# Kernel tuning notes

Hardware: AMD Instinct MI355X
Metric: run time of the kernel (lower is better)

Reference implementation:

```python
import jax, jax.numpy as jnp
import numpy as np
import jax.lax as lax


def _log_bf_np(z, s2, s0):
    # Bayes factor per feature; s0 is the prior precision tau_0[l,k] (scalar)
    s0_inv = 1.0 / s0
    s2ps0inv = s2 + s0_inv
    return 0.5 * (jnp.log(s2) - jnp.log(s2ps0inv) + z ** 2 * (s0_inv / s2ps0inv))


def setup_inputs() -> dict:
    key = jax.random.key(0)
    ks = jax.random.split(key, 8)
    n, p, z, l = 1000, 50000, 20, 10
    data = jax.random.normal(ks[0], (n, p), jnp.float32)
    mean_z = jax.random.normal(ks[1], (n, z), jnp.float32)
    # factor second moment must be PSD with strictly positive diagonal (E_zzk > 0)
    mean_zz = (mean_z.T @ mean_z) / n + jnp.eye(z, dtype=jnp.float32)
    mean_w = jax.random.normal(ks[2], (l, z, p), jnp.float32) * 0.01
    var_w = jax.random.uniform(ks[3], (l, z), jnp.float32, minval=0.1, maxval=1.0)
    alpha = jax.random.uniform(ks[4], (l, z, p), jnp.float32)
    alpha = alpha / jnp.sum(alpha, axis=-1, keepdims=True)
    tau = jnp.asarray(1.5, jnp.float32)
    tau_0 = jax.random.uniform(ks[5], (l, z), jnp.float32, minval=0.5, maxval=2.0)
    pi = jax.random.uniform(ks[6], (z, p), jnp.float32, minval=0.5, maxval=1.5)
    pi = pi / jnp.sum(pi, axis=-1, keepdims=True)
    return {"data": data, "mean_z": mean_z, "mean_zz": mean_zz, "mean_w": mean_w,
            "var_w": var_w, "alpha": alpha, "tau": tau, "tau_0": tau_0, "pi": pi}


def reference(data, mean_z, mean_zz, mean_w, var_w, alpha, tau, tau_0, pi):
    """LoadingModel.update: sequential CAVI over factors (k) and single effects (l).
    mean_w/alpha: [l, z, p]; var_w/tau_0: [l, z]; pi: [z, p]; data: [n, p]; mean_z: [n, z].
    Returns updated (mean_w, var_w, alpha)."""
    l_dim, z_dim, p_dim = mean_w.shape
    # collapsed loading moments: W[k, :] = sum_l mean_w[l,k,:] * alpha[l,k,:]
    W = jnp.sum(mean_w * alpha, axis=0)            # [z, p]
    ZtX = mean_z.T @ data                           # [z, p] (precompute of mean_z[:,k] @ data)
    log_pi = jnp.log(pi)                            # [z, p]

    def factor_step(carry, kdx):
        W, mean_w, var_w, alpha = carry
        E_zzk = mean_zz[kdx, kdx]
        Wk = W[kdx]                                 # [p]
        # Wnk.T @ E_zpzk over j != k  ==  mean_zz[kdx] @ W - E_zzk * Wk (avoids the gather)
        RtZk = ZtX[kdx] - (mean_zz[kdx] @ W - E_zzk * Wk)   # [p]
        log_pi_k = log_pi[kdx]
        s2_s = 1.0 / (E_zzk * tau)
        zs_scale = jnp.sqrt(E_zzk * tau) / E_zzk

        def effect_step(Wk, xs):
            mw_l, a_l, t0_l = xs                    # [p], [p], scalar
            Wkl = Wk - mw_l * a_l                   # remove effect l from residual fit
            E_RtZk = RtZk - E_zzk * Wkl             # [p]
            var_new = jnp.reciprocal(tau * E_zzk + t0_l)   # scalar
            mean_new = tau * var_new * E_RtZk       # [p]
            Z_s = E_RtZk * zs_scale
            log_bf = _log_bf_np(Z_s, s2_s, t0_l)
            alpha_new = jax.nn.softmax(log_pi_k + log_bf)
            Wk_new = Wkl + mean_new * alpha_new
            return Wk_new, (mean_new, var_new, alpha_new)

        Wk_new, (mw_rows, vw_rows, a_rows) = lax.scan(
            effect_step, Wk, (mean_w[:, kdx, :], alpha[:, kdx, :], tau_0[:, kdx]))
        mean_w = mean_w.at[:, kdx, :].set(mw_rows)
        var_w = var_w.at[:, kdx].set(vw_rows)
        alpha = alpha.at[:, kdx, :].set(a_rows)
        W = W.at[kdx].set(Wk_new)
        return (W, mean_w, var_w, alpha), None

    (W, mean_w, var_w, alpha), _ = lax.scan(
        factor_step, (W, mean_w, var_w, alpha), jnp.arange(z_dim))
    return mean_w, var_w, alpha
```

## Files before the change

kernel.cpp:

```cpp
#include <hip/hip_runtime.h>
#include <stdint.h>


#define NTHREADS 256
#define NBLK 196
constexpr int N_DIM = 1000;
constexpr int P_DIM = 50000;
constexpr int Z_DIM = 20;
constexpr int L_DIM = 10;

using u64 = unsigned long long;

__device__ __forceinline__ float wred_max(float v) {
#pragma unroll
  for (int m = 32; m; m >>= 1) v = fmaxf(v, __shfl_xor(v, m, 64));
  return v;
}
__device__ __forceinline__ float wred_sum(float v) {
#pragma unroll
  for (int m = 32; m; m >>= 1) v += __shfl_xor(v, m, 64);
  return v;
}

__global__ __launch_bounds__(NTHREADS) void loading_model_kernel(
    const float* __restrict__ data,
    const float* __restrict__ mean_z,
    const float* __restrict__ mean_zz,
    const float* __restrict__ mean_w_in,
    const float* __restrict__ alpha_in,
    const float* __restrict__ tau_p,
    const float* __restrict__ tau0,
    const float* __restrict__ pi,
    float* __restrict__ out_mw,
    float* __restrict__ out_vw,
    float* __restrict__ out_alpha,
    u64* __restrict__ ws)
{
  const int tid  = threadIdx.x;
  const int blk  = blockIdx.x;
  const int gid  = blk * NTHREADS + tid;
  const bool active = (gid < P_DIM);
  const int lane = tid & 63;
  const int wid  = tid >> 6;
  const float tau = tau_p[0];

  __shared__ float lds_wmax[4];
  __shared__ float lds_wsum[4];
  __shared__ float lds_lse;

  if (blk == 0 && tid < L_DIM * Z_DIM) {
    int k = tid % Z_DIM;
    float E = mean_zz[k * Z_DIM + k];
    out_vw[tid] = 1.0f / (tau * E + tau0[tid]);
  }

  float ztx[Z_DIM];
#pragma unroll
  for (int k = 0; k < Z_DIM; k++) ztx[k] = 0.f;
  {
    const float* dcol = data + gid;
#pragma unroll 8
    for (int n = 0; n < N_DIM; n++) {
      float d = active ? dcol[(size_t)n * P_DIM] : 0.f;
#pragma unroll
      for (int k = 0; k < Z_DIM; k++) ztx[k] += mean_z[n * Z_DIM + k] * d;
    }
  }

  float W[Z_DIM];
#pragma unroll
  for (int j = 0; j < Z_DIM; j++) W[j] = 0.f;
  for (int l = 0; l < L_DIM; l++) {
#pragma unroll
    for (int j = 0; j < Z_DIM; j++) {
      if (active) {
        size_t idx = ((size_t)(l * Z_DIM + j)) * P_DIM + gid;
        W[j] += mean_w_in[idx] * alpha_in[idx];
      }
    }
  }

  u64* slots  = ws;
  u64* result = ws + 2 * NBLK;

  float pival = active ? pi[gid] : 1.0f;
  float mw = 0.f, av = 0.f;
  if (active) { mw = mean_w_in[gid]; av = alpha_in[gid]; }

#pragma unroll
  for (int k = 0; k < Z_DIM; k++) {
    const float E    = mean_zz[k * Z_DIM + k];
    const float ktau = tau * E;
    const float s2   = 1.0f / ktau;
    const float zsc2 = tau / E;

    float acc = 0.f;
#pragma unroll
    for (int j = 0; j < Z_DIM; j++) acc += mean_zz[k * Z_DIM + j] * W[j];
    const float RtZk = ztx[k] - (acc - E * W[k]);
    const float lpk  = active ? __logf(pival) : -INFINITY;
    if (k + 1 < Z_DIM && active) pival = pi[(size_t)(k + 1) * P_DIM + gid];

    float Wk = W[k];
    for (int l = 0; l < L_DIM; l++) {
      const float t0    = tau0[l * Z_DIM + k];
      const float s0inv = 1.0f / t0;
      const float s2p   = s2 + s0inv;
      const float c0    = 0.5f * (__logf(s2) - __logf(s2p));
      const float c1    = 0.5f * zsc2 * (s0inv / s2p);
      const float varn  = 1.0f / (ktau + t0);
      const float mnc   = tau * varn;

      const float Wkl = Wk - mw * av;
      const float E_R = RtZk - E * Wkl;
      const float mean_new = mnc * E_R;
      float logit = lpk + c0 + c1 * E_R * E_R;
      if (!active) logit = -INFINITY;

      const size_t oidx = ((size_t)(l * Z_DIM + k)) * P_DIM + gid;
      if (active) out_mw[oidx] = mean_new;

      float mw_n = 0.f, av_n = 0.f;
      {
        int ln = l + 1, kn = k;
        if (ln == L_DIM) { ln = 0; kn = k + 1; }
        if (kn < Z_DIM && active) {
          size_t idx2 = ((size_t)(ln * Z_DIM + kn)) * P_DIM + gid;
          mw_n = mean_w_in[idx2];
          av_n = alpha_in[idx2];
        }
      }

      float wmax = wred_max(logit);
      float ew   = active ? __expf(logit - wmax) : 0.f;
      float wsum = wred_sum(ew);
      if (lane == 0) { lds_wmax[wid] = wmax; lds_wsum[wid] = wsum; }
      __syncthreads();

      const int s   = k * L_DIM + l + 1;
      const int buf = s & 1;
      if (tid == 0) {
        float m0 = lds_wmax[0], m1 = lds_wmax[1];
        float m2 = lds_wmax[2], m3 = lds_wmax[3];
        float M4 = fmaxf(fmaxf(m0, m1), fmaxf(m2, m3));
        float S4 = __expf(m0 - M4) * lds_wsum[0] + __expf(m1 - M4) * lds_wsum[1]
                 + __expf(m2 - M4) * lds_wsum[2] + __expf(m3 - M4) * lds_wsum[3];
        float lse_b = M4 + __logf(S4);
        __hip_atomic_store(&slots[buf * NBLK + blk],
                           (((u64)(unsigned)s) << 32) | (u64)__float_as_uint(lse_b),
                           __ATOMIC_RELAXED, __HIP_MEMORY_SCOPE_AGENT);
      }

      if (wid == 0) {
        if (blk == 0) {
          u64 raw[4];
          bool ok = false;
          while (!ok) {
            ok = true;
#pragma unroll
            for (int q = 0; q < 4; q++) {
              int j = lane + (q << 6);
              if (j < NBLK)
                raw[q] = __hip_atomic_load(&slots[buf * NBLK + j],
                                           __ATOMIC_RELAXED, __HIP_MEMORY_SCOPE_AGENT);
            }
#pragma unroll
            for (int q = 0; q < 4; q++) {
              int j = lane + (q << 6);
              if (j < NBLK && (unsigned)(raw[q] >> 32) != (unsigned)s) ok = false;
            }
          }
          float m = -INFINITY;
#pragma unroll
          for (int q = 0; q < 4; q++) {
            int j = lane + (q << 6);
            if (j < NBLK) m = fmaxf(m, __uint_as_float((unsigned)raw[q]));
          }
          float M = wred_max(m);
          float ps = 0.f;
#pragma unroll
          for (int q = 0; q < 4; q++) {
            int j = lane + (q << 6);
            if (j < NBLK) ps += __expf(__uint_as_float((unsigned)raw[q]) - M);
          }
          float S = wred_sum(ps);
          float LSE = M + __logf(S);
          if (lane == 0) {
            __hip_atomic_store(&result[buf],
                               (((u64)(unsigned)s) << 32) | (u64)__float_as_uint(LSE),
                               __ATOMIC_RELAXED, __HIP_MEMORY_SCOPE_AGENT);
            lds_lse = LSE;
          }
        } else if (lane == 0) {
          u64 v;
          do {
            v = __hip_atomic_load(&result[buf],
                                  __ATOMIC_RELAXED, __HIP_MEMORY_SCOPE_AGENT);
          } while ((unsigned)(v >> 32) != (unsigned)s);
          lds_lse = __uint_as_float((unsigned)v);
        }
      }
      __syncthreads();

      const float LSEt = lds_lse;
      const float alpha_new = active ? __expf(logit - LSEt) : 0.f;
      Wk = Wkl + mean_new * alpha_new;
      if (active) out_alpha[oidx] = alpha_new;
      mw = mw_n;
      av = av_n;
    }
    W[k] = Wk;
  }
}

extern "C" void kernel_launch(void* const* d_in, const int* in_sizes, int n_in,
                              void* d_out, int out_size, void* d_ws, size_t ws_size,
                              hipStream_t stream) {
  const float* data    = (const float*)d_in[0];
  const float* mean_z  = (const float*)d_in[1];
  const float* mean_zz = (const float*)d_in[2];
  const float* mean_w  = (const float*)d_in[3];
  const float* alpha   = (const float*)d_in[5];
  const float* tau     = (const float*)d_in[6];
  const float* tau0    = (const float*)d_in[7];
  const float* pi      = (const float*)d_in[8];

  float* out_mw    = (float*)d_out;
  float* out_vw    = out_mw + (size_t)L_DIM * Z_DIM * P_DIM;
  float* out_alpha = out_vw + (size_t)L_DIM * Z_DIM;
  u64*   ws        = (u64*)d_ws;

  hipMemsetAsync(d_ws, 0, (2 * NBLK + 2) * sizeof(u64), stream);

  void* args[] = {(void*)&data, (void*)&mean_z, (void*)&mean_zz, (void*)&mean_w,
                  (void*)&alpha, (void*)&tau, (void*)&tau0, (void*)&pi,
                  (void*)&out_mw, (void*)&out_vw, (void*)&out_alpha, (void*)&ws};
  hipLaunchCooperativeKernel((void*)loading_model_kernel, dim3(NBLK),
                             dim3(NTHREADS), args, 0, stream);
}
```

Before: 1.355 ms.

## Replace two-hop grid LSE reduction with all-blocks redundant slot reduction

Each of the 200 sequential softmax steps used to wait for block 0 to gather every per-block partial log-sum-exp and publish a global result, which all other blocks then polled. Now every block's first wave polls all per-block slots itself and computes the global LSE locally, removing the second cross-block hop from each step. The polling loop remembers which slots have already arrived. The next step's scalar constants and the mean_w/alpha prefetch are moved into the window between publishing a partial and waiting for the others, so they overlap the wait. The cost is heavier global-memory polling traffic, since all 196 blocks now read every slot.

```diff
diff --git a/kernel.cpp b/kernel.cpp
--- a/kernel.cpp
+++ b/kernel.cpp
@@ -80,19 +80,30 @@
     }
   }
 
-  u64* slots  = ws;
-  u64* result = ws + 2 * NBLK;
+  u64* slots = ws;
 
   float pival = active ? pi[gid] : 1.0f;
   float mw = 0.f, av = 0.f;
   if (active) { mw = mean_w_in[gid]; av = alpha_in[gid]; }
 
+  const float E0    = mean_zz[0];
+  const float ktau0 = tau * E0;
+  float cs2   = 1.0f / ktau0;
+  float czsc2 = tau / E0;
+  float nc0, nc1, nmnc;
+  {
+    const float t0    = tau0[0];
+    const float s0inv = 1.0f / t0;
+    const float s2p   = cs2 + s0inv;
+    nc0  = 0.5f * (__logf(cs2) - __logf(s2p));
+    nc1  = 0.5f * czsc2 * (s0inv / s2p);
+    nmnc = tau / (ktau0 + t0);
+  }
+
 #pragma unroll
   for (int k = 0; k < Z_DIM; k++) {
     const float E    = mean_zz[k * Z_DIM + k];
     const float ktau = tau * E;
-    const float s2   = 1.0f / ktau;
-    const float zsc2 = tau / E;
 
     float acc = 0.f;
 #pragma unroll
@@ -103,13 +114,9 @@
 
     float Wk = W[k];
     for (int l = 0; l < L_DIM; l++) {
-      const float t0    = tau0[l * Z_DIM + k];
-      const float s0inv = 1.0f / t0;
-      const float s2p   = s2 + s0inv;
-      const float c0    = 0.5f * (__logf(s2) - __logf(s2p));
-      const float c1    = 0.5f * zsc2 * (s0inv / s2p);
-      const float varn  = 1.0f / (ktau + t0);
-      const float mnc   = tau * varn;
+      const float c0  = nc0;
+      const float c1  = nc1;
+      const float mnc = nmnc;
 
       const float Wkl = Wk - mw * av;
       const float E_R = RtZk - E * Wkl;
@@ -119,17 +126,6 @@
 
       const size_t oidx = ((size_t)(l * Z_DIM + k)) * P_DIM + gid;
       if (active) out_mw[oidx] = mean_new;
-
-      float mw_n = 0.f, av_n = 0.f;
-      {
-        int ln = l + 1, kn = k;
-        if (ln == L_DIM) { ln = 0; kn = k + 1; }
-        if (kn < Z_DIM && active) {
-          size_t idx2 = ((size_t)(ln * Z_DIM + kn)) * P_DIM + gid;
-          mw_n = mean_w_in[idx2];
-          av_n = alpha_in[idx2];
-        }
-      }
 
       float wmax = wred_max(logit);
       float ew   = active ? __expf(logit - wmax) : 0.f;
@@ -151,54 +147,70 @@
                            __ATOMIC_RELAXED, __HIP_MEMORY_SCOPE_AGENT);
       }
 
+      float mw_n = 0.f, av_n = 0.f;
+      {
+        int ln = l + 1, kn = k;
+        if (ln == L_DIM) { ln = 0; kn = k + 1; }
+        if (kn < Z_DIM) {
+          if (active) {
+            size_t idx2 = ((size_t)(ln * Z_DIM + kn)) * P_DIM + gid;
+            mw_n = mean_w_in[idx2];
+            av_n = alpha_in[idx2];
+          }
+          if (ln == 0) {
+            const float En = mean_zz[kn * Z_DIM + kn];
+            const float kt = tau * En;
+            cs2   = 1.0f / kt;
+            czsc2 = tau / En;
+          }
+          const float t0n   = tau0[ln * Z_DIM + kn];
+          const float s0inv = 1.0f / t0n;
+          const float s2p   = cs2 + s0inv;
+          nc0  = 0.5f * (__logf(cs2) - __logf(s2p));
+          nc1  = 0.5f * czsc2 * (s0inv / s2p);
+          nmnc = (ln == 0) ? tau / (tau * mean_zz[kn * Z_DIM + kn] + t0n)
+                           : tau / (ktau + t0n);
+        }
+      }
+
       if (wid == 0) {
-        if (blk == 0) {
-          u64 raw[4];
-          bool ok = false;
-          while (!ok) {
-            ok = true;
-#pragma unroll
-            for (int q = 0; q < 4; q++) {
-              int j = lane + (q << 6);
-              if (j < NBLK)
-                raw[q] = __hip_atomic_load(&slots[buf * NBLK + j],
-                                           __ATOMIC_RELAXED, __HIP_MEMORY_SCOPE_AGENT);
-            }
-#pragma unroll
-            for (int q = 0; q < 4; q++) {
-              int j = lane + (q << 6);
-              if (j < NBLK && (unsigned)(raw[q] >> 32) != (unsigned)s) ok = false;
-            }
-          }
-          float m = -INFINITY;
+        u64 raw[4];
+        bool need[4];
+#pragma unroll
+        for (int q = 0; q < 4; q++) need[q] = (lane + (q << 6)) < NBLK;
+        bool pend = true;
+        while (pend) {
 #pragma unroll
           for (int q = 0; q < 4; q++) {
             int j = lane + (q << 6);
-            if (j < NBLK) m = fmaxf(m, __uint_as_float((unsigned)raw[q]));
-          }
-          float M = wred_max(m);
-          float ps = 0.f;
+            if (need[q])
+              raw[q] = __hip_atomic_load(&slots[buf * NBLK + j],
+                                         __ATOMIC_RELAXED, __HIP_MEMORY_SCOPE_AGENT);
+          }
+          pend = false;
 #pragma unroll
           for (int q = 0; q < 4; q++) {
-            int j = lane + (q << 6);
-            if (j < NBLK) ps += __expf(__uint_as_float((unsigned)raw[q]) - M);
-          }
-          float S = wred_sum(ps);
-          float LSE = M + __logf(S);
-          if (lane == 0) {
-            __hip_atomic_store(&result[buf],
-                               (((u64)(unsigned)s) << 32) | (u64)__float_as_uint(LSE),
-                               __ATOMIC_RELAXED, __HIP_MEMORY_SCOPE_AGENT);
-            lds_lse = LSE;
-          }
-        } else if (lane == 0) {
-          u64 v;
-          do {
-            v = __hip_atomic_load(&result[buf],
-                                  __ATOMIC_RELAXED, __HIP_MEMORY_SCOPE_AGENT);
-          } while ((unsigned)(v >> 32) != (unsigned)s);
-          lds_lse = __uint_as_float((unsigned)v);
-        }
+            if (need[q]) {
+              if ((unsigned)(raw[q] >> 32) == (unsigned)s) need[q] = false;
+              else pend = true;
+            }
+          }
+        }
+        float m = -INFINITY;
+#pragma unroll
+        for (int q = 0; q < 4; q++) {
+          int j = lane + (q << 6);
+          if (j < NBLK) m = fmaxf(m, __uint_as_float((unsigned)raw[q]));
+        }
+        float M = wred_max(m);
+        float ps = 0.f;
+#pragma unroll
+        for (int q = 0; q < 4; q++) {
+          int j = lane + (q << 6);
+          if (j < NBLK) ps += __expf(__uint_as_float((unsigned)raw[q]) - M);
+        }
+        float S = wred_sum(ps);
+        if (lane == 0) lds_lse = M + __logf(S);
       }
       __syncthreads();
 
@@ -230,7 +242,7 @@
   float* out_alpha = out_vw + (size_t)L_DIM * Z_DIM;
   u64*   ws        = (u64*)d_ws;
 
-  hipMemsetAsync(d_ws, 0, (2 * NBLK + 2) * sizeof(u64), stream);
+  hipMemsetAsync(d_ws, 0, 2 * NBLK * sizeof(u64), stream);
 
   void* args[] = {(void*)&data, (void*)&mean_z, (void*)&mean_zz, (void*)&mean_w,
                   (void*)&alpha, (void*)&tau, (void*)&tau0, (void*)&pi,
```

Result: no change. 1.344 ms (-0.9%).
